# Kernel tuning notes

Hardware: AMD Instinct MI355X
Metric: run time of the kernel (lower is better)

Reference implementation:

```python
import jax, jax.numpy as jnp
import numpy as np

N, E, IN, HID, ADIM, EDIM, H = 20000, 320000, 128, 128, 16, 16, 2


def _lin(key, out_d, in_d, scale=0.05):
    kw, kb = jax.random.split(key)
    W = jax.random.normal(kw, (out_d, in_d), jnp.float32) * scale
    b = jax.random.normal(kb, (out_d,), jnp.float32) * scale
    return W, b


def _gat_params(key):
    k = jax.random.split(key, 4)
    Wl, bl = _lin(k[0], H * HID, HID)
    Wr, br = _lin(k[1], H * HID, HID)
    We = jax.random.normal(k[2], (H * HID, EDIM), jnp.float32) * 0.05  # lin_edge, no bias
    att = jax.random.normal(k[3], (1, H, HID), jnp.float32) * 0.05
    bias = jnp.zeros((HID,), jnp.float32)  # concat=False -> out bias of size HID
    return Wl, bl, Wr, br, We, att, bias


def setup_inputs() -> dict:
    key = jax.random.key(0)
    ks = jax.random.split(key, 16)
    inp = {}
    inp['x'] = jax.random.normal(ks[0], (N, IN), jnp.float32)
    inp['edge_index'] = jax.random.randint(ks[1], (2, E), 0, N, jnp.int64 if jax.config.jax_enable_x64 else jnp.int32)
    inp['edge_attr'] = jax.random.normal(ks[2], (E, EDIM), jnp.float32)
    inp['action'] = jax.random.normal(ks[3], (N, ADIM), jnp.float32)
    inp['inp_W'], inp['inp_b'] = _lin(ks[4], HID, IN)
    for i, name in enumerate(['s1', 's2', 'sa']):
        Wl, bl, Wr, br, We, att, bias = _gat_params(ks[5 + i])
        inp[f'{name}_Wl'], inp[f'{name}_bl'] = Wl, bl
        inp[f'{name}_Wr'], inp[f'{name}_br'] = Wr, br
        inp[f'{name}_We'], inp[f'{name}_att'], inp[f'{name}_bias'] = We, att, bias
    inp['ap_W'], inp['ap_b'] = _lin(ks[8], HID, ADIM)
    inp['g_W'], inp['g_b'] = _lin(ks[9], HID, HID)
    inp['be_W'], inp['be_b'] = _lin(ks[10], HID, HID)
    inp['q1_W'], inp['q1_b'] = _lin(ks[11], HID, HID)
    inp['q2_W'], inp['q2_b'] = _lin(ks[12], 1, HID)
    return inp


def gatv2(h, src, dst, ea, Wl, bl, Wr, br, We, att, bias):
    """PyG GATv2Conv, heads=H, concat=False (mean over heads), with edge_attr."""
    n = h.shape[0]
    xl = (h @ Wl.T + bl).reshape(n, H, HID)   # source transform
    xr = (h @ Wr.T + br).reshape(n, H, HID)   # destination transform
    em = (ea @ We.T).reshape(-1, H, HID)      # [E,H,C]
    m = jax.nn.leaky_relu(xl[src] + xr[dst] + em, 0.2)   # [E,H,C]
    logit = (m * att).sum(-1)                 # [E,H]
    lmax = jax.ops.segment_max(logit, dst, num_segments=n)
    w = jnp.exp(logit - lmax[dst])
    den = jax.ops.segment_sum(w, dst, num_segments=n)
    alpha = w / den[dst]                      # segment softmax over incoming edges
    out = jax.ops.segment_sum(alpha[..., None] * xl[src], dst, num_segments=n)  # [n,H,C]
    return out.mean(axis=1) + bias


def reference(x, edge_index, edge_attr, action, inp_W, inp_b,
              s1_Wl, s1_bl, s1_Wr, s1_br, s1_We, s1_att, s1_bias,
              s2_Wl, s2_bl, s2_Wr, s2_br, s2_We, s2_att, s2_bias,
              sa_Wl, sa_bl, sa_Wr, sa_br, sa_We, sa_att, sa_bias,
              ap_W, ap_b, g_W, g_b, be_W, be_b, q1_W, q1_b, q2_W, q2_b):
    src, dst = edge_index[0], edge_index[1]
    h = jax.nn.relu(x @ inp_W.T + inp_b)
    h = jax.nn.relu(gatv2(h, src, dst, edge_attr, s1_Wl, s1_bl, s1_Wr, s1_br, s1_We, s1_att, s1_bias))
    h = jax.nn.relu(gatv2(h, src, dst, edge_attr, s2_Wl, s2_bl, s2_Wr, s2_br, s2_We, s2_att, s2_bias))
    a = jax.nn.relu(action @ ap_W.T + ap_b)
    h = (a @ g_W.T + g_b) * h + (a @ be_W.T + be_b)   # FiLM modulation
    h = jax.nn.relu(gatv2(h, src, dst, edge_attr, sa_Wl, sa_bl, sa_Wr, sa_br, sa_We, sa_att, sa_bias))
    h = jax.nn.relu(h @ q1_W.T + q1_b)
    q_node = h @ q2_W.T + q2_b                         # [N,1]
    return q_node.mean(axis=0, keepdims=True)          # [1,1]
```

## Files before the change

### kernel.cpp

```cpp
#include <hip/hip_runtime.h>
#include <hip/hip_bf16.h>


typedef __attribute__((ext_vector_type(8))) short bf16x8;
typedef __attribute__((ext_vector_type(4))) float f32x4;
typedef __attribute__((ext_vector_type(2))) float f32x2;

__device__ __forceinline__ unsigned short f2bf(float f) {
    union { float f; unsigned int i; } v; v.f = f;
    unsigned int x = v.i;
    x += 0x7fffu + ((x >> 16) & 1u);
    return (unsigned short)(x >> 16);
}
__device__ __forceinline__ float4 b4f(ushort4 u) {
    union { unsigned int i; float f; } a, b, c, d;
    a.i = (unsigned int)u.x << 16; b.i = (unsigned int)u.y << 16;
    c.i = (unsigned int)u.z << 16; d.i = (unsigned int)u.w << 16;
    return make_float4(a.f, b.f, c.f, d.f);
}
__device__ __forceinline__ unsigned char f2fp8(float f) {
    return (unsigned char)(__builtin_amdgcn_cvt_pk_fp8_f32(f, f, 0, false) & 0xFF);
}

#define MAXCVT 12
struct CvtDescs {
    const float* src[MAXCVT];
    unsigned short* dst[MAXCVT];
    int n4[MAXCVT];
    int cnt;
};
__global__ __launch_bounds__(256) void cvt_many_kernel(CvtDescs d) {
    const int tid = blockIdx.x * blockDim.x + threadIdx.x;
    const int stride = gridDim.x * blockDim.x;
    for (int e = 0; e < d.cnt; ++e) {
        const float4* s = (const float4*)d.src[e];
        ushort4* o = (ushort4*)d.dst[e];
        const int n = d.n4[e];
        for (int i = tid; i < n; i += stride) {
            float4 v = s[i];
            o[i] = make_ushort4(f2bf(v.x), f2bf(v.y), f2bf(v.z), f2bf(v.w));
        }
    }
}

struct PadDescs {
    const float* src[4];
    unsigned short* dst[4];
    int rows[4];
    int cnt;
};
__global__ __launch_bounds__(256) void cvt_pad_kernel(PadDescs d) {
    const int tid = blockIdx.x * blockDim.x + threadIdx.x;
    const int stride = gridDim.x * blockDim.x;
    const ushort4 z = make_ushort4(0, 0, 0, 0);
    for (int e = 0; e < d.cnt; ++e) {
        const float4* s = (const float4*)d.src[e];
        ushort4* o = (ushort4*)d.dst[e];
        const int rows = d.rows[e];
        for (int r = tid; r < rows; r += stride) {
            const float4* sp = s + (size_t)r * 4;
            ushort4* op = o + (size_t)r * 8;
#pragma unroll
            for (int q = 0; q < 4; ++q) {
                float4 v = sp[q];
                op[q] = make_ushort4(f2bf(v.x), f2bf(v.y), f2bf(v.z), f2bf(v.w));
            }
#pragma unroll
            for (int q = 4; q < 8; ++q) op[q] = z;
        }
    }
}

__global__ void hist_kernel(const int* __restrict__ dst, int* __restrict__ deg, int n) {
    int i = blockIdx.x * blockDim.x + threadIdx.x;
    if (i < n) atomicAdd(&deg[dst[i]], 1);
}

__global__ __launch_bounds__(1024) void scan_kernel(const int* __restrict__ deg,
                                                    int* __restrict__ rowp,
                                                    int* __restrict__ cur, int n) {
    __shared__ int sums[1024];
    const int t = threadIdx.x;
    const int PER = 20;
    int base = t * PER;
    int local[PER];
    int run = 0;
#pragma unroll
    for (int i = 0; i < PER; ++i) {
        int v = (base + i < n) ? deg[base + i] : 0;
        local[i] = run; run += v;
    }
    sums[t] = run; __syncthreads();
    for (int off = 1; off < 1024; off <<= 1) {
        int v = (t >= off) ? sums[t - off] : 0;
        __syncthreads();
        sums[t] += v;
        __syncthreads();
    }
    int offs = (t > 0) ? sums[t - 1] : 0;
#pragma unroll
    for (int i = 0; i < PER; ++i) {
        int idx = base + i;
        if (idx < n) { int v = offs + local[i]; rowp[idx] = v; cur[idx] = v; }
    }
    if (t == 0) rowp[n] = sums[1023];
}

__global__ void scatter_kernel(const int* __restrict__ src, const int* __restrict__ dst,
                               int* __restrict__ cur, const float4* __restrict__ ea,
                               int* __restrict__ csrs, int* __restrict__ csrd,
                               ushort4* __restrict__ eacsr, int n) {
    int i = blockIdx.x * blockDim.x + threadIdx.x;
    if (i < n) {
        int d = dst[i];
        int p = atomicAdd(&cur[d], 1);
        csrs[p] = src[i];
        csrd[p] = d;
        const float4* er = ea + (size_t)i * 4;
        ushort4* eo = eacsr + (size_t)p * 8;
        const ushort4 z = make_ushort4(0, 0, 0, 0);
#pragma unroll
        for (int q = 0; q < 4; ++q) {
            float4 v = er[q];
            eo[q] = make_ushort4(f2bf(v.x), f2bf(v.y), f2bf(v.z), f2bf(v.w));
        }
#pragma unroll
        for (int q = 4; q < 8; ++q) eo[q] = z;
    }
}

template <bool RELU, bool SPLIT>
__global__ __launch_bounds__(256) void gemm_mfma_kernel(
    const unsigned short* __restrict__ A, const unsigned short* __restrict__ W,
    const float* __restrict__ bias0, const float* __restrict__ bias1, int bsplit,
    unsigned short* __restrict__ Cbf, unsigned char* __restrict__ Cf8,
    int M, int N, int K) {
    const int t = threadIdx.x;
    const int wave = t >> 6, lane = t & 63;
    const int lo = lane & 15, quad = lane >> 4;
    const int m0 = blockIdx.y * 128 + wave * 32;
    const int n0 = blockIdx.x * 64;

    f32x4 acc[2][4];
#pragma unroll
    for (int i = 0; i < 2; ++i)
#pragma unroll
        for (int j = 0; j < 4; ++j) acc[i][j] = (f32x4){0.f, 0.f, 0.f, 0.f};

    for (int k0 = 0; k0 < K; k0 += 32) {
        bf16x8 af[2], bfr[4];
#pragma unroll
        for (int mi = 0; mi < 2; ++mi) {
            const int mb = m0 + mi * 16;
            af[mi] = (mb < M) ? *(const bf16x8*)(A + (size_t)(mb + lo) * K + k0 + quad * 8)
                              : (bf16x8){0, 0, 0, 0, 0, 0, 0, 0};
        }
#pragma unroll
        for (int ni = 0; ni < 4; ++ni)
            bfr[ni] = *(const bf16x8*)(W + (size_t)(n0 + ni * 16 + lo) * K + k0 + quad * 8);
#pragma unroll
        for (int mi = 0; mi < 2; ++mi)
#pragma unroll
            for (int ni = 0; ni < 4; ++ni)
                acc[mi][ni] = __builtin_amdgcn_mfma_f32_16x16x32_bf16(af[mi], bfr[ni], acc[mi][ni], 0, 0, 0);
    }

    float bn[4];
#pragma unroll
    for (int ni = 0; ni < 4; ++ni) {
        const int n = n0 + ni * 16 + lo;
        const float* bp = (n < bsplit) ? bias0 : bias1;
        const int bi = (n < bsplit) ? n : n - bsplit;
        bn[ni] = bp[bi];
    }
#pragma unroll
    for (int mi = 0; mi < 2; ++mi) {
        const int mb = m0 + mi * 16;
        if (mb >= M) continue;
#pragma unroll
        for (int ni = 0; ni < 4; ++ni) {
            const int n = n0 + ni * 16 + lo;
#pragma unroll
            for (int r = 0; r < 4; ++r) {
                float o = acc[mi][ni][r] + bn[ni];
                if (RELU) o = fmaxf(o, 0.f);
                const int row = mb + quad * 4 + r;
                if (SPLIT) {
                    if (n < 256) Cbf[(size_t)row * 256 + n] = f2bf(o);
                    Cf8[(size_t)row * 512 + n] = f2fp8(o);
                } else {
                    Cbf[(size_t)row * N + n] = f2bf(o);
                }
            }
        }
    }
}

__global__ __launch_bounds__(256) void gemm_film_kernel(
    const unsigned short* __restrict__ A, const unsigned short* __restrict__ Wg,
    const unsigned short* __restrict__ Wb, const float* __restrict__ gb,
    const float* __restrict__ bb, unsigned short* __restrict__ hbf, int M) {
    const int K = 128, N = 128;
    const int t = threadIdx.x;
    const int wave = t >> 6, lane = t & 63;
    const int lo = lane & 15, quad = lane >> 4;
    const int m0 = blockIdx.y * 128 + wave * 32;
    const int n0 = blockIdx.x * 64;

    f32x4 accg[2][4], accb[2][4];
#pragma unroll
    for (int i = 0; i < 2; ++i)
#pragma unroll
        for (int j = 0; j < 4; ++j) { accg[i][j] = (f32x4){0.f,0.f,0.f,0.f}; accb[i][j] = accg[i][j]; }

    for (int k0 = 0; k0 < K; k0 += 32) {
        bf16x8 af[2], bg4[4];
#pragma unroll
        for (int mi = 0; mi < 2; ++mi) {
            const int mb = m0 + mi * 16;
            af[mi] = (mb < M) ? *(const bf16x8*)(A + (size_t)(mb + lo) * K + k0 + quad * 8)
                              : (bf16x8){0,0,0,0,0,0,0,0};
        }
#pragma unroll
        for (int ni = 0; ni < 4; ++ni)
            bg4[ni] = *(const bf16x8*)(Wg + (size_t)(n0 + ni * 16 + lo) * K + k0 + quad * 8);
#pragma unroll
        for (int mi = 0; mi < 2; ++mi)
#pragma unroll
            for (int ni = 0; ni < 4; ++ni)
                accg[mi][ni] = __builtin_amdgcn_mfma_f32_16x16x32_bf16(af[mi], bg4[ni], accg[mi][ni], 0, 0, 0);
#pragma unroll
        for (int ni = 0; ni < 4; ++ni)
            bg4[ni] = *(const bf16x8*)(Wb + (size_t)(n0 + ni * 16 + lo) * K + k0 + quad * 8);
#pragma unroll
        for (int mi = 0; mi < 2; ++mi)
#pragma unroll
            for (int ni = 0; ni < 4; ++ni)
                accb[mi][ni] = __builtin_amdgcn_mfma_f32_16x16x32_bf16(af[mi], bg4[ni], accb[mi][ni], 0, 0, 0);
    }

#pragma unroll
    for (int mi = 0; mi < 2; ++mi) {
        const int mb = m0 + mi * 16;
        if (mb >= M) continue;
#pragma unroll
        for (int ni = 0; ni < 4; ++ni) {
            const int n = n0 + ni * 16 + lo;
            const float g = gb[n], b = bb[n];
#pragma unroll
            for (int r = 0; r < 4; ++r) {
                const size_t idx = (size_t)(mb + quad * 4 + r) * N + n;
                union { unsigned int i; float f; } hv; hv.i = (unsigned int)hbf[idx] << 16;
                hbf[idx] = f2bf((accg[mi][ni][r] + g) * hv.f + (accb[mi][ni][r] + b));
            }
        }
    }
}

__global__ __launch_bounds__(256) void gemm_q1_kernel(
    const unsigned short* __restrict__ A, const unsigned short* __restrict__ W,
    const float* __restrict__ q1b, const float* __restrict__ q2w,
    float* __restrict__ outsum, int M) {
    const int K = 128;
    const int t = threadIdx.x;
    const int wave = t >> 6, lane = t & 63;
    const int lo = lane & 15, quad = lane >> 4;
    const int m0 = blockIdx.y * 128 + wave * 32;
    const int n0 = blockIdx.x * 64;
    __shared__ float red[4];

    f32x4 acc[2][4];
#pragma unroll
    for (int i = 0; i < 2; ++i)
#pragma unroll
        for (int j = 0; j < 4; ++j) acc[i][j] = (f32x4){0.f, 0.f, 0.f, 0.f};

    for (int k0 = 0; k0 < K; k0 += 32) {
        bf16x8 af[2], bfr[4];
#pragma unroll
        for (int mi = 0; mi < 2; ++mi) {
            const int mb = m0 + mi * 16;
            af[mi] = (mb < M) ? *(const bf16x8*)(A + (size_t)(mb + lo) * K + k0 + quad * 8)
                              : (bf16x8){0,0,0,0,0,0,0,0};
        }
#pragma unroll
        for (int ni = 0; ni < 4; ++ni)
            bfr[ni] = *(const bf16x8*)(W + (size_t)(n0 + ni * 16 + lo) * K + k0 + quad * 8);
#pragma unroll
        for (int mi = 0; mi < 2; ++mi)
#pragma unroll
            for (int ni = 0; ni < 4; ++ni)
                acc[mi][ni] = __builtin_amdgcn_mfma_f32_16x16x32_bf16(af[mi], bfr[ni], acc[mi][ni], 0, 0, 0);
    }

    float partial = 0.f;
#pragma unroll
    for (int mi = 0; mi < 2; ++mi) {
        const int mb = m0 + mi * 16;
        if (mb >= M) continue;
#pragma unroll
        for (int ni = 0; ni < 4; ++ni) {
            const int n = n0 + ni * 16 + lo;
            const float b = q1b[n], w = q2w[n];
#pragma unroll
            for (int r = 0; r < 4; ++r)
                partial += fmaxf(acc[mi][ni][r] + b, 0.f) * w;
        }
    }
    partial += __shfl_xor(partial, 1);  partial += __shfl_xor(partial, 2);
    partial += __shfl_xor(partial, 4);  partial += __shfl_xor(partial, 8);
    partial += __shfl_xor(partial, 16); partial += __shfl_xor(partial, 32);
    if (lane == 0) red[wave] = partial;
    __syncthreads();
    if (t == 0) atomicAdd(outsum, red[0] + red[1] + red[2] + red[3]);
}

template <int BK, bool RELU, bool WBF16>
__global__ __launch_bounds__(256) void gemm_kernel(const float* __restrict__ A,
                                                   const float* __restrict__ W,
                                                   const float* __restrict__ bp,
                                                   float* __restrict__ C,
                                                   unsigned short* __restrict__ Cbf,
                                                   int M, int N, int K) {
    __shared__ float As[BK][68];
    __shared__ float Ws[BK][68];
    const int t = threadIdx.x;
    const int m0 = blockIdx.y * 64;
    const int n0 = blockIdx.x * 64;
    const int tx = t & 15, ty = t >> 4;
    float acc[4][4];
#pragma unroll
    for (int i = 0; i < 4; ++i)
#pragma unroll
        for (int j = 0; j < 4; ++j) acc[i][j] = 0.f;

    for (int k0 = 0; k0 < K; k0 += BK) {
        const int r = t >> 2, cc = (t & 3) * 4;
        const int arow = m0 + r;
        float4 av = (arow < M) ? *(const float4*)(A + (size_t)arow * K + k0 + cc)
                               : make_float4(0.f, 0.f, 0.f, 0.f);
        As[cc + 0][r] = av.x; As[cc + 1][r] = av.y;
        As[cc + 2][r] = av.z; As[cc + 3][r] = av.w;
        float4 wv = *(const float4*)(W + (size_t)(n0 + r) * K + k0 + cc);
        Ws[cc + 0][r] = wv.x; Ws[cc + 1][r] = wv.y;
        Ws[cc + 2][r] = wv.z; Ws[cc + 3][r] = wv.w;
        __syncthreads();
#pragma unroll
        for (int k = 0; k < BK; ++k) {
            float4 a4 = *(const float4*)&As[k][ty * 4];
            float4 b4 = *(const float4*)&Ws[k][tx * 4];
            float a_[4] = {a4.x, a4.y, a4.z, a4.w};
            float b_[4] = {b4.x, b4.y, b4.z, b4.w};
#pragma unroll
            for (int i = 0; i < 4; ++i)
#pragma unroll
                for (int j = 0; j < 4; ++j) acc[i][j] += a_[i] * b_[j];
        }
        __syncthreads();
    }
    float4 bj = *(const float4*)(bp + n0 + tx * 4);
    float bb[4] = {bj.x, bj.y, bj.z, bj.w};
#pragma unroll
    for (int i = 0; i < 4; ++i) {
        int row = m0 + ty * 4 + i;
        if (row < M) {
            float o[4];
#pragma unroll
            for (int j = 0; j < 4; ++j) {
                o[j] = acc[i][j] + bb[j];
                if (RELU) o[j] = fmaxf(o[j], 0.f);
            }
            *(float4*)(C + (size_t)row * N + n0 + tx * 4) = make_float4(o[0], o[1], o[2], o[3]);
            if (WBF16)
                *(ushort4*)(Cbf + (size_t)row * N + n0 + tx * 4) =
                    make_ushort4(f2bf(o[0]), f2bf(o[1]), f2bf(o[2]), f2bf(o[3]));
        }
    }
}

#define LSTR 272
__global__ __launch_bounds__(256, 4) void gat_logit_kernel(
    const unsigned char* __restrict__ xf8,
    const int* __restrict__ csrs, const int* __restrict__ csrd,
    const unsigned short* __restrict__ eacsr, const unsigned short* __restrict__ wepad,
    const float* __restrict__ att, float* __restrict__ logit, int E) {
    __shared__ float attl[256];
    __shared__ __align__(16) unsigned char xls[4][16 * LSTR];
    __shared__ __align__(16) unsigned char xrs[4][16 * LSTR];
    const int tid = threadIdx.x;
    attl[tid] = att[tid];
    const int wave = tid >> 6, lane = tid & 63;
    const int lo = lane & 15, quad = lane >> 4;
    const int sr_row = lane >> 2, c16 = (lane & 3) * 16;

    bf16x8 wef[16];
#pragma unroll
    for (int t = 0; t < 16; ++t)
        wef[t] = *(const bf16x8*)(wepad + (size_t)(t * 16 + lo) * 32 + quad * 8);

    const int nb = (E + 15) / 16;
    const int wstride = gridDim.x * 4;
    const int trips = (nb + wstride - 1) / wstride;
    for (int it = 0; it < trips; ++it) {
        const int b = blockIdx.x * 4 + wave + it * wstride;
        const bool vb = b < nb;
        const int p0 = vb ? b * 16 : 0;
        if (vb) {
            const int pr = min(p0 + sr_row, E - 1);
            const int sr = csrs[pr], dr = csrd[pr];
            const unsigned char* xs = xf8 + (size_t)sr * 512 + c16;
            const unsigned char* xrp = xf8 + (size_t)dr * 512 + 256 + c16;
            unsigned char* ld = &xls[wave][sr_row * LSTR + c16];
            unsigned char* rd = &xrs[wave][sr_row * LSTR + c16];
#pragma unroll
            for (int j = 0; j < 4; ++j) {
                *(int4*)(ld + j * 64) = *(const int4*)(xs + j * 64);
                *(int4*)(rd + j * 64) = *(const int4*)(xrp + j * 64);
            }
        }
        __syncthreads();
        if (vb) {
            const bool valid = (p0 + lo) < E;
            const int p = valid ? (p0 + lo) : (E - 1);
            const bf16x8 eaf = *(const bf16x8*)(eacsr + (size_t)p * 32 + quad * 8);
            float ph0 = 0.f, ph1 = 0.f;
#pragma unroll
            for (int t = 0; t < 16; ++t) {
                f32x4 D = __builtin_amdgcn_mfma_f32_16x16x32_bf16(
                    wef[t], eaf, (f32x4){0.f, 0.f, 0.f, 0.f}, 0, 0, 0);
                const int c0 = t * 16 + quad * 4;
                const unsigned int xlu = *(const unsigned int*)&xls[wave][lo * LSTR + c0];
                const unsigned int xru = *(const unsigned int*)&xrs[wave][lo * LSTR + c0];
                const f32x2 l01 = __builtin_amdgcn_cvt_pk_f32_fp8(xlu, false);
                const f32x2 l23 = __builtin_amdgcn_cvt_pk_f32_fp8(xlu, true);
                const f32x2 r01 = __builtin_amdgcn_cvt_pk_f32_fp8(xru, false);
                const f32x2 r23 = __builtin_amdgcn_cvt_pk_f32_fp8(xru, true);
                const float4 at4 = *(const float4*)&attl[c0];
                float vx = l01.x + r01.x + D[0];
                float vy = l01.y + r01.y + D[1];
                float vz = l23.x + r23.x + D[2];
                float vw = l23.y + r23.y + D[3];
                vx = fmaxf(vx, 0.2f * vx); vy = fmaxf(vy, 0.2f * vy);
                vz = fmaxf(vz, 0.2f * vz); vw = fmaxf(vw, 0.2f * vw);
                const float pt = vx * at4.x + vy * at4.y + vz * at4.z + vw * at4.w;
                if (t < 8) ph0 += pt; else ph1 += pt;
            }
            ph0 += __shfl_xor(ph0, 16); ph0 += __shfl_xor(ph0, 32);
            ph1 += __shfl_xor(ph1, 16); ph1 += __shfl_xor(ph1, 32);
            if (valid) {
                if (quad == 0) logit[p0 + lo] = ph0;
                else if (quad == 1) logit[(size_t)E + p0 + lo] = ph1;
            }
        }
        __syncthreads();
    }
}

__global__ __launch_bounds__(256) void gat_na_kernel(
    const unsigned short* __restrict__ xlb,
    const int* __restrict__ rowp, const int* __restrict__ csrs,
    const float* __restrict__ wgt, const float* __restrict__ bias,
    unsigned short* __restrict__ houtb, int nnodes, int E) {
    const int lane = threadIdx.x & 63;
    const int node = blockIdx.x * 4 + (threadIdx.x >> 6);
    if (node >= nnodes) return;
    const int rs = rowp[node], re = rowp[node + 1];
    const int h = lane >> 5, l = lane & 31;
    const float* lg = wgt + (size_t)h * E;

    float mx = -INFINITY;
    for (int i = rs + l; i < re; i += 32) mx = fmaxf(mx, lg[i]);
    mx = fmaxf(mx, __shfl_xor(mx, 1));  mx = fmaxf(mx, __shfl_xor(mx, 2));
    mx = fmaxf(mx, __shfl_xor(mx, 4));  mx = fmaxf(mx, __shfl_xor(mx, 8));
    mx = fmaxf(mx, __shfl_xor(mx, 16));
    float sum = 0.f;
    for (int i = rs + l; i < re; i += 32) sum += __expf(lg[i] - mx);
    sum += __shfl_xor(sum, 1);  sum += __shfl_xor(sum, 2);  sum += __shfl_xor(sum, 4);
    sum += __shfl_xor(sum, 8);  sum += __shfl_xor(sum, 16);
    const float inv = (re > rs) ? 1.f / sum : 0.f;

    float4 acc0 = make_float4(0.f, 0.f, 0.f, 0.f), acc1 = acc0;
    int i = rs;
    for (; i + 1 < re; i += 2) {
        const int s0 = csrs[i], s1 = csrs[i + 1];
        const float w0 = __expf(lg[i] - mx) * inv;
        const float w1 = __expf(lg[i + 1] - mx) * inv;
        const float4 x0 = b4f(*(const ushort4*)(xlb + (size_t)s0 * 256 + 4 * lane));
        const float4 x1 = b4f(*(const ushort4*)(xlb + (size_t)s1 * 256 + 4 * lane));
        acc0.x += w0 * x0.x; acc0.y += w0 * x0.y; acc0.z += w0 * x0.z; acc0.w += w0 * x0.w;
        acc1.x += w1 * x1.x; acc1.y += w1 * x1.y; acc1.z += w1 * x1.z; acc1.w += w1 * x1.w;
    }
    if (i < re) {
        const int s0 = csrs[i];
        const float w0 = __expf(lg[i] - mx) * inv;
        const float4 x0 = b4f(*(const ushort4*)(xlb + (size_t)s0 * 256 + 4 * lane));
        acc0.x += w0 * x0.x; acc0.y += w0 * x0.y; acc0.z += w0 * x0.z; acc0.w += w0 * x0.w;
    }
    float ox = acc0.x + acc1.x, oy = acc0.y + acc1.y;
    float oz = acc0.z + acc1.z, ow = acc0.w + acc1.w;
    ox += __shfl_xor(ox, 32); oy += __shfl_xor(oy, 32);
    oz += __shfl_xor(oz, 32); ow += __shfl_xor(ow, 32);
    if (lane < 32) {
        float4 bu = *(const float4*)(bias + 4 * lane);
        *(ushort4*)(houtb + (size_t)node * 128 + 4 * lane) = make_ushort4(
            f2bf(fmaxf(0.5f * ox + bu.x, 0.f)), f2bf(fmaxf(0.5f * oy + bu.y, 0.f)),
            f2bf(fmaxf(0.5f * oz + bu.z, 0.f)), f2bf(fmaxf(0.5f * ow + bu.w, 0.f)));
    }
}

__global__ void final_kernel(const float* __restrict__ s, const float* __restrict__ q2b,
                             float* __restrict__ out, float invn) {
    out[0] = s[0] * invn + q2b[0];
}

extern "C" void kernel_launch(void* const* d_in, const int* in_sizes, int n_in,
                              void* d_out, int out_size, void* d_ws, size_t ws_size,
                              hipStream_t stream) {
    const int N = in_sizes[0] / 128;
    const int E = in_sizes[1] / 2;

    typedef const float* fp;
    fp x      = (fp)d_in[0];
    const int* ei = (const int*)d_in[1];
    fp ea     = (fp)d_in[2];
    fp action = (fp)d_in[3];
    fp inp_W  = (fp)d_in[4];
    fp inp_b  = (fp)d_in[5];
    fp ap_W = (fp)d_in[27], ap_b = (fp)d_in[28];
    fp g_W  = (fp)d_in[29], g_b  = (fp)d_in[30];
    fp be_W = (fp)d_in[31], be_b = (fp)d_in[32];
    fp q1_W = (fp)d_in[33], q1_b = (fp)d_in[34];
    fp q2_W = (fp)d_in[35], q2_b = (fp)d_in[36];

    char* base = (char*)d_ws;
    size_t off = 0;
    auto alloc = [&](size_t bytes) { char* p = base + off; off = (off + bytes + 255) & ~(size_t)255; return p; };
    unsigned short* xfb = (unsigned short*)alloc((size_t)N * 256 * 2);
    unsigned char*  xf8 = (unsigned char*)alloc((size_t)N * 512);
    float* col  = (float*)alloc(128 * 4);
    int* deg    = (int*)alloc((size_t)N * 4);
    int* rowp   = (int*)alloc((size_t)(N + 1) * 4);
    int* cur    = (int*)alloc((size_t)N * 4);
    int* csrs   = (int*)alloc((size_t)E * 4);
    int* csrd   = (int*)alloc((size_t)E * 4);
    unsigned short* eacsr = (unsigned short*)alloc((size_t)E * 32 * 2);
    float* wgt  = (float*)alloc((size_t)2 * E * 4);
    unsigned short* hbf = (unsigned short*)alloc((size_t)N * 128 * 2);
    unsigned short* xbf = (unsigned short*)alloc((size_t)N * 128 * 2);
    unsigned short* wbf = (unsigned short*)alloc((262144 + 3 * 8192) * 2);
    float* abuf = (float*)xfb;
    unsigned short* abf = xbf;
    (void)ws_size; (void)n_in; (void)out_size;

    unsigned short* winp = wbf;
    unsigned short* w1l  = wbf + 16384;
    unsigned short* w1r  = w1l + 32768;
    unsigned short* w2l  = w1r + 32768;
    unsigned short* w2r  = w2l + 32768;
    unsigned short* wal  = w2r + 32768;
    unsigned short* war  = wal + 32768;
    unsigned short* wg   = war + 32768;
    unsigned short* wbe  = wg + 16384;
    unsigned short* wq1  = wbe + 16384;
    unsigned short* wep1 = wq1 + 16384;
    unsigned short* wep2 = wep1 + 8192;
    unsigned short* wep3 = wep2 + 8192;

    const int* src = ei;
    const int* dst = ei + E;

    CvtDescs cd;
    int ce = 0;
    auto addc = [&](const float* s, unsigned short* d, int n) { cd.src[ce] = s; cd.dst[ce] = d; cd.n4[ce] = n / 4; ++ce; };
    addc(x, xbf, N * 128);
    addc(inp_W, winp, 16384);
    addc((fp)d_in[6],  w1l, 32768); addc((fp)d_in[8],  w1r, 32768);
    addc((fp)d_in[13], w2l, 32768); addc((fp)d_in[15], w2r, 32768);
    addc((fp)d_in[20], wal, 32768); addc((fp)d_in[22], war, 32768);
    addc(g_W, wg, 16384); addc(be_W, wbe, 16384); addc(q1_W, wq1, 16384);
    cd.cnt = ce;
    cvt_many_kernel<<<2048, 256, 0, stream>>>(cd);

    PadDescs pd;
    pd.src[0] = (fp)d_in[10]; pd.dst[0] = wep1; pd.rows[0] = 256;
    pd.src[1] = (fp)d_in[17]; pd.dst[1] = wep2; pd.rows[1] = 256;
    pd.src[2] = (fp)d_in[24]; pd.dst[2] = wep3; pd.rows[2] = 256;
    pd.cnt = 3;
    cvt_pad_kernel<<<64, 256, 0, stream>>>(pd);

    hipMemsetAsync(deg, 0, (size_t)N * 4, stream);
    hist_kernel<<<(E + 255) / 256, 256, 0, stream>>>(dst, deg, E);
    scan_kernel<<<1, 1024, 0, stream>>>(deg, rowp, cur, N);
    scatter_kernel<<<(E + 255) / 256, 256, 0, stream>>>(src, dst, cur, (const float4*)ea,
                                                        csrs, csrd, (ushort4*)eacsr, E);

    const int my = (N + 127) / 128;
    const int nodeg = (N + 3) / 4;

    auto run_gat = [&](const unsigned short* wep, const float* at, const float* bi,
                       unsigned short* hb) {
        gat_logit_kernel<<<2048, 256, 0, stream>>>(xf8, csrs, csrd, eacsr, wep, at, wgt, E);
        gat_na_kernel<<<nodeg, 256, 0, stream>>>(xfb, rowp, csrs, wgt, bi, hb, N, E);
    };

    gemm_mfma_kernel<true, false><<<dim3(2, my), 256, 0, stream>>>(
        xbf, winp, inp_b, inp_b, 128, hbf, nullptr, N, 128, 128);

    gemm_mfma_kernel<false, true><<<dim3(8, my), 256, 0, stream>>>(
        hbf, w1l, (fp)d_in[7], (fp)d_in[9], 256, xfb, xf8, N, 512, 128);
    run_gat(wep1, (fp)d_in[11], (fp)d_in[12], hbf);
    gemm_mfma_kernel<false, true><<<dim3(8, my), 256, 0, stream>>>(
        hbf, w2l, (fp)d_in[14], (fp)d_in[16], 256, xfb, xf8, N, 512, 128);
    run_gat(wep2, (fp)d_in[18], (fp)d_in[19], hbf);

    gemm_kernel<16, true, true><<<dim3(2, (N + 63) / 64), 256, 0, stream>>>(
        action, ap_W, ap_b, abuf, abf, N, 128, 16);
    gemm_film_kernel<<<dim3(2, my), 256, 0, stream>>>(abf, wg, wbe, g_b, be_b, hbf, N);

    gemm_mfma_kernel<false, true><<<dim3(8, my), 256, 0, stream>>>(
        hbf, wal, (fp)d_in[21], (fp)d_in[23], 256, xfb, xf8, N, 512, 128);
    run_gat(wep3, (fp)d_in[25], (fp)d_in[26], hbf);

    hipMemsetAsync(col, 0, 4, stream);
    gemm_q1_kernel<<<dim3(2, my), 256, 0, stream>>>(hbf, wq1, q1_b, q2_W, col, N);
    final_kernel<<<1, 1, 0, stream>>>(col, q2_b, (float*)d_out, 1.0f / (float)N);
}
```

Measured before the change: 500.0 us.

## Aggregate from fp8 source features and drop bf16 copies and padded edge buffers

The neighbor aggregation kernel now gathers source features from the fp8 buffer the GEMM already writes, using the packed fp8-to-f32 convert. This removes the separate bf16 copy of the transformed features and its write traffic. Edge attributes and edge weights are stored unpadded, with 16 instead of 32 columns. Zeros are supplied in registers, so the scatter writes half as much and the separate padding kernel is removed. The unused fp32 output of the action GEMM is also dropped. The trade-off is lower precision in the aggregated messages, since fp8 has only a 3-bit mantissa.

```diff
diff --git a/kernel.cpp b/kernel.cpp
--- a/kernel.cpp
+++ b/kernel.cpp
@@ -5,6 +5,8 @@
 typedef __attribute__((ext_vector_type(8))) short bf16x8;
 typedef __attribute__((ext_vector_type(4))) float f32x4;
 typedef __attribute__((ext_vector_type(2))) float f32x2;
+
+#define ZERO8 ((bf16x8){0, 0, 0, 0, 0, 0, 0, 0})
 
 __device__ __forceinline__ unsigned short f2bf(float f) {
     union { float f; unsigned int i; } v; v.f = f;
@@ -12,17 +14,11 @@
     x += 0x7fffu + ((x >> 16) & 1u);
     return (unsigned short)(x >> 16);
 }
-__device__ __forceinline__ float4 b4f(ushort4 u) {
-    union { unsigned int i; float f; } a, b, c, d;
-    a.i = (unsigned int)u.x << 16; b.i = (unsigned int)u.y << 16;
-    c.i = (unsigned int)u.z << 16; d.i = (unsigned int)u.w << 16;
-    return make_float4(a.f, b.f, c.f, d.f);
-}
 __device__ __forceinline__ unsigned char f2fp8(float f) {
     return (unsigned char)(__builtin_amdgcn_cvt_pk_fp8_f32(f, f, 0, false) & 0xFF);
 }
 
-#define MAXCVT 12
+#define MAXCVT 16
 struct CvtDescs {
     const float* src[MAXCVT];
     unsigned short* dst[MAXCVT];
@@ -43,34 +39,6 @@
     }
 }
 
-struct PadDescs {
-    const float* src[4];
-    unsigned short* dst[4];
-    int rows[4];
-    int cnt;
-};
-__global__ __launch_bounds__(256) void cvt_pad_kernel(PadDescs d) {
-    const int tid = blockIdx.x * blockDim.x + threadIdx.x;
-    const int stride = gridDim.x * blockDim.x;
-    const ushort4 z = make_ushort4(0, 0, 0, 0);
-    for (int e = 0; e < d.cnt; ++e) {
-        const float4* s = (const float4*)d.src[e];
-        ushort4* o = (ushort4*)d.dst[e];
-        const int rows = d.rows[e];
-        for (int r = tid; r < rows; r += stride) {
-            const float4* sp = s + (size_t)r * 4;
-            ushort4* op = o + (size_t)r * 8;
-#pragma unroll
-            for (int q = 0; q < 4; ++q) {
-                float4 v = sp[q];
-                op[q] = make_ushort4(f2bf(v.x), f2bf(v.y), f2bf(v.z), f2bf(v.w));
-            }
-#pragma unroll
-            for (int q = 4; q < 8; ++q) op[q] = z;
-        }
-    }
-}
-
 __global__ void hist_kernel(const int* __restrict__ dst, int* __restrict__ deg, int n) {
     int i = blockIdx.x * blockDim.x + threadIdx.x;
     if (i < n) atomicAdd(&deg[dst[i]], 1);
@@ -117,15 +85,12 @@
         csrs[p] = src[i];
         csrd[p] = d;
         const float4* er = ea + (size_t)i * 4;
-        ushort4* eo = eacsr + (size_t)p * 8;
-        const ushort4 z = make_ushort4(0, 0, 0, 0);
+        ushort4* eo = eacsr + (size_t)p * 4;
 #pragma unroll
         for (int q = 0; q < 4; ++q) {
             float4 v = er[q];
             eo[q] = make_ushort4(f2bf(v.x), f2bf(v.y), f2bf(v.z), f2bf(v.w));
         }
-#pragma unroll
-        for (int q = 4; q < 8; ++q) eo[q] = z;
     }
 }
 
@@ -153,7 +118,7 @@
         for (int mi = 0; mi < 2; ++mi) {
             const int mb = m0 + mi * 16;
             af[mi] = (mb < M) ? *(const bf16x8*)(A + (size_t)(mb + lo) * K + k0 + quad * 8)
-                              : (bf16x8){0, 0, 0, 0, 0, 0, 0, 0};
+                              : ZERO8;
         }
 #pragma unroll
         for (int ni = 0; ni < 4; ++ni)
@@ -185,12 +150,8 @@
                 float o = acc[mi][ni][r] + bn[ni];
                 if (RELU) o = fmaxf(o, 0.f);
                 const int row = mb + quad * 4 + r;
-                if (SPLIT) {
-                    if (n < 256) Cbf[(size_t)row * 256 + n] = f2bf(o);
-                    Cf8[(size_t)row * 512 + n] = f2fp8(o);
-                } else {
-                    Cbf[(size_t)row * N + n] = f2bf(o);
-                }
+                if (SPLIT) Cf8[(size_t)row * 512 + n] = f2fp8(o);
+                else       Cbf[(size_t)row * N + n] = f2bf(o);
             }
         }
     }
@@ -219,7 +180,7 @@
         for (int mi = 0; mi < 2; ++mi) {
             const int mb = m0 + mi * 16;
             af[mi] = (mb < M) ? *(const bf16x8*)(A + (size_t)(mb + lo) * K + k0 + quad * 8)
-                              : (bf16x8){0,0,0,0,0,0,0,0};
+                              : ZERO8;
         }
 #pragma unroll
         for (int ni = 0; ni < 4; ++ni)
@@ -281,7 +242,7 @@
         for (int mi = 0; mi < 2; ++mi) {
             const int mb = m0 + mi * 16;
             af[mi] = (mb < M) ? *(const bf16x8*)(A + (size_t)(mb + lo) * K + k0 + quad * 8)
-                              : (bf16x8){0,0,0,0,0,0,0,0};
+                              : ZERO8;
         }
 #pragma unroll
         for (int ni = 0; ni < 4; ++ni)
@@ -315,11 +276,10 @@
     if (t == 0) atomicAdd(outsum, red[0] + red[1] + red[2] + red[3]);
 }
 
-template <int BK, bool RELU, bool WBF16>
+template <int BK, bool RELU>
 __global__ __launch_bounds__(256) void gemm_kernel(const float* __restrict__ A,
                                                    const float* __restrict__ W,
                                                    const float* __restrict__ bp,
-                                                   float* __restrict__ C,
                                                    unsigned short* __restrict__ Cbf,
                                                    int M, int N, int K) {
     __shared__ float As[BK][68];
@@ -370,10 +330,8 @@
                 o[j] = acc[i][j] + bb[j];
                 if (RELU) o[j] = fmaxf(o[j], 0.f);
             }
-            *(float4*)(C + (size_t)row * N + n0 + tx * 4) = make_float4(o[0], o[1], o[2], o[3]);
-            if (WBF16)
-                *(ushort4*)(Cbf + (size_t)row * N + n0 + tx * 4) =
-                    make_ushort4(f2bf(o[0]), f2bf(o[1]), f2bf(o[2]), f2bf(o[3]));
+            *(ushort4*)(Cbf + (size_t)row * N + n0 + tx * 4) =
+                make_ushort4(f2bf(o[0]), f2bf(o[1]), f2bf(o[2]), f2bf(o[3]));
         }
     }
 }
@@ -382,7 +340,7 @@
 __global__ __launch_bounds__(256, 4) void gat_logit_kernel(
     const unsigned char* __restrict__ xf8,
     const int* __restrict__ csrs, const int* __restrict__ csrd,
-    const unsigned short* __restrict__ eacsr, const unsigned short* __restrict__ wepad,
+    const unsigned short* __restrict__ eacsr, const unsigned short* __restrict__ we16,
     const float* __restrict__ att, float* __restrict__ logit, int E) {
     __shared__ float attl[256];
     __shared__ __align__(16) unsigned char xls[4][16 * LSTR];
@@ -396,7 +354,8 @@
     bf16x8 wef[16];
 #pragma unroll
     for (int t = 0; t < 16; ++t)
-        wef[t] = *(const bf16x8*)(wepad + (size_t)(t * 16 + lo) * 32 + quad * 8);
+        wef[t] = (quad < 2) ? *(const bf16x8*)(we16 + (size_t)(t * 16 + lo) * 16 + quad * 8)
+                            : ZERO8;
 
     const int nb = (E + 15) / 16;
     const int wstride = gridDim.x * 4;
@@ -422,7 +381,8 @@
         if (vb) {
             const bool valid = (p0 + lo) < E;
             const int p = valid ? (p0 + lo) : (E - 1);
-            const bf16x8 eaf = *(const bf16x8*)(eacsr + (size_t)p * 32 + quad * 8);
+            const bf16x8 eaf = (quad < 2)
+                ? *(const bf16x8*)(eacsr + (size_t)p * 16 + quad * 8) : ZERO8;
             float ph0 = 0.f, ph1 = 0.f;
 #pragma unroll
             for (int t = 0; t < 16; ++t) {
@@ -457,7 +417,7 @@
 }
 
 __global__ __launch_bounds__(256) void gat_na_kernel(
-    const unsigned short* __restrict__ xlb,
+    const unsigned char* __restrict__ xf8,
     const int* __restrict__ rowp, const int* __restrict__ csrs,
     const float* __restrict__ wgt, const float* __restrict__ bias,
     unsigned short* __restrict__ houtb, int nnodes, int E) {
@@ -485,16 +445,22 @@
         const int s0 = csrs[i], s1 = csrs[i + 1];
         const float w0 = __expf(lg[i] - mx) * inv;
         const float w1 = __expf(lg[i + 1] - mx) * inv;
-        const float4 x0 = b4f(*(const ushort4*)(xlb + (size_t)s0 * 256 + 4 * lane));
-        const float4 x1 = b4f(*(const ushort4*)(xlb + (size_t)s1 * 256 + 4 * lane));
-        acc0.x += w0 * x0.x; acc0.y += w0 * x0.y; acc0.z += w0 * x0.z; acc0.w += w0 * x0.w;
-        acc1.x += w1 * x1.x; acc1.y += w1 * x1.y; acc1.z += w1 * x1.z; acc1.w += w1 * x1.w;
+        const unsigned int u0 = *(const unsigned int*)(xf8 + (size_t)s0 * 512 + 4 * lane);
+        const unsigned int u1 = *(const unsigned int*)(xf8 + (size_t)s1 * 512 + 4 * lane);
+        const f32x2 a01 = __builtin_amdgcn_cvt_pk_f32_fp8(u0, false);
+        const f32x2 a23 = __builtin_amdgcn_cvt_pk_f32_fp8(u0, true);
+        const f32x2 b01 = __builtin_amdgcn_cvt_pk_f32_fp8(u1, false);
+        const f32x2 b23 = __builtin_amdgcn_cvt_pk_f32_fp8(u1, true);
+        acc0.x += w0 * a01.x; acc0.y += w0 * a01.y; acc0.z += w0 * a23.x; acc0.w += w0 * a23.y;
+        acc1.x += w1 * b01.x; acc1.y += w1 * b01.y; acc1.z += w1 * b23.x; acc1.w += w1 * b23.y;
     }
     if (i < re) {
         const int s0 = csrs[i];
         const float w0 = __expf(lg[i] - mx) * inv;
-        const float4 x0 = b4f(*(const ushort4*)(xlb + (size_t)s0 * 256 + 4 * lane));
-        acc0.x += w0 * x0.x; acc0.y += w0 * x0.y; acc0.z += w0 * x0.z; acc0.w += w0 * x0.w;
+        const unsigned int u0 = *(const unsigned int*)(xf8 + (size_t)s0 * 512 + 4 * lane);
+        const f32x2 a01 = __builtin_amdgcn_cvt_pk_f32_fp8(u0, false);
+        const f32x2 a23 = __builtin_amdgcn_cvt_pk_f32_fp8(u0, true);
+        acc0.x += w0 * a01.x; acc0.y += w0 * a01.y; acc0.z += w0 * a23.x; acc0.w += w0 * a23.y;
     }
     float ox = acc0.x + acc1.x, oy = acc0.y + acc1.y;
     float oz = acc0.z + acc1.z, ow = acc0.w + acc1.w;
@@ -535,7 +501,6 @@
     char* base = (char*)d_ws;
     size_t off = 0;
     auto alloc = [&](size_t bytes) { char* p = base + off; off = (off + bytes + 255) & ~(size_t)255; return p; };
-    unsigned short* xfb = (unsigned short*)alloc((size_t)N * 256 * 2);
     unsigned char*  xf8 = (unsigned char*)alloc((size_t)N * 512);
     float* col  = (float*)alloc(128 * 4);
     int* deg    = (int*)alloc((size_t)N * 4);
@@ -543,12 +508,11 @@
     int* cur    = (int*)alloc((size_t)N * 4);
     int* csrs   = (int*)alloc((size_t)E * 4);
     int* csrd   = (int*)alloc((size_t)E * 4);
-    unsigned short* eacsr = (unsigned short*)alloc((size_t)E * 32 * 2);
+    unsigned short* eacsr = (unsigned short*)alloc((size_t)E * 16 * 2);
     float* wgt  = (float*)alloc((size_t)2 * E * 4);
     unsigned short* hbf = (unsigned short*)alloc((size_t)N * 128 * 2);
     unsigned short* xbf = (unsigned short*)alloc((size_t)N * 128 * 2);
-    unsigned short* wbf = (unsigned short*)alloc((262144 + 3 * 8192) * 2);
-    float* abuf = (float*)xfb;
+    unsigned short* wbf = (unsigned short*)alloc((262144 + 3 * 4096) * 2);
     unsigned short* abf = xbf;
     (void)ws_size; (void)n_in; (void)out_size;
 
@@ -563,8 +527,8 @@
     unsigned short* wbe  = wg + 16384;
     unsigned short* wq1  = wbe + 16384;
     unsigned short* wep1 = wq1 + 16384;
-    unsigned short* wep2 = wep1 + 8192;
-    unsigned short* wep3 = wep2 + 8192;
+    unsigned short* wep2 = wep1 + 4096;
+    unsigned short* wep3 = wep2 + 4096;
 
     const int* src = ei;
     const int* dst = ei + E;
@@ -578,15 +542,9 @@
     addc((fp)d_in[13], w2l, 32768); addc((fp)d_in[15], w2r, 32768);
     addc((fp)d_in[20], wal, 32768); addc((fp)d_in[22], war, 32768);
     addc(g_W, wg, 16384); addc(be_W, wbe, 16384); addc(q1_W, wq1, 16384);
+    addc((fp)d_in[10], wep1, 4096); addc((fp)d_in[17], wep2, 4096); addc((fp)d_in[24], wep3, 4096);
     cd.cnt = ce;
     cvt_many_kernel<<<2048, 256, 0, stream>>>(cd);
-
-    PadDescs pd;
-    pd.src[0] = (fp)d_in[10]; pd.dst[0] = wep1; pd.rows[0] = 256;
-    pd.src[1] = (fp)d_in[17]; pd.dst[1] = wep2; pd.rows[1] = 256;
-    pd.src[2] = (fp)d_in[24]; pd.dst[2] = wep3; pd.rows[2] = 256;
-    pd.cnt = 3;
-    cvt_pad_kernel<<<64, 256, 0, stream>>>(pd);
 
     hipMemsetAsync(deg, 0, (size_t)N * 4, stream);
     hist_kernel<<<(E + 255) / 256, 256, 0, stream>>>(dst, deg, E);
@@ -600,25 +558,25 @@
     auto run_gat = [&](const unsigned short* wep, const float* at, const float* bi,
                        unsigned short* hb) {
         gat_logit_kernel<<<2048, 256, 0, stream>>>(xf8, csrs, csrd, eacsr, wep, at, wgt, E);
-        gat_na_kernel<<<nodeg, 256, 0, stream>>>(xfb, rowp, csrs, wgt, bi, hb, N, E);
+        gat_na_kernel<<<nodeg, 256, 0, stream>>>(xf8, rowp, csrs, wgt, bi, hb, N, E);
     };
 
     gemm_mfma_kernel<true, false><<<dim3(2, my), 256, 0, stream>>>(
         xbf, winp, inp_b, inp_b, 128, hbf, nullptr, N, 128, 128);
 
     gemm_mfma_kernel<false, true><<<dim3(8, my), 256, 0, stream>>>(
-        hbf, w1l, (fp)d_in[7], (fp)d_in[9], 256, xfb, xf8, N, 512, 128);
+        hbf, w1l, (fp)d_in[7], (fp)d_in[9], 256, nullptr, xf8, N, 512, 128);
     run_gat(wep1, (fp)d_in[11], (fp)d_in[12], hbf);
     gemm_mfma_kernel<false, true><<<dim3(8, my), 256, 0, stream>>>(
-        hbf, w2l, (fp)d_in[14], (fp)d_in[16], 256, xfb, xf8, N, 512, 128);
+        hbf, w2l, (fp)d_in[14], (fp)d_in[16], 256, nullptr, xf8, N, 512, 128);
     run_gat(wep2, (fp)d_in[18], (fp)d_in[19], hbf);
 
-    gemm_kernel<16, true, true><<<dim3(2, (N + 63) / 64), 256, 0, stream>>>(
-        action, ap_W, ap_b, abuf, abf, N, 128, 16);
+    gemm_kernel<16, true><<<dim3(2, (N + 63) / 64), 256, 0, stream>>>(
+        action, ap_W, ap_b, abf, N, 128, 16);
     gemm_film_kernel<<<dim3(2, my), 256, 0, stream>>>(abf, wg, wbe, g_b, be_b, hbf, N);
 
     gemm_mfma_kernel<false, true><<<dim3(8, my), 256, 0, stream>>>(
-        hbf, wal, (fp)d_in[21], (fp)d_in[23], 256, xfb, xf8, N, 512, 128);
+        hbf, wal, (fp)d_in[21], (fp)d_in[23], 256, nullptr, xf8, N, 512, 128);
     run_gat(wep3, (fp)d_in[25], (fp)d_in[26], hbf);
 
     hipMemsetAsync(col, 0, 4, stream);
```

Result: faster. 469.3 us (-6.1%).
